# Kernel tuning notes

Measured on AMD Instinct MI355X. Metric: run time of the kernel, lower is better.

## Reference

```python
import jax, jax.numpy as jnp
import numpy as np
from jax import lax


def setup_inputs() -> dict:
    key = jax.random.key(0)
    k1, k2 = jax.random.split(key)
    C, H, W = 64, 224, 224
    C_out, hf, wf = 128, 3, 3
    x = jax.random.normal(k1, (C, H, W), dtype=jnp.float32)
    kernels = jax.random.normal(k2, (C_out, C, hf, wf), dtype=jnp.float32)
    return {"x": x, "kernels": kernels}


def reference(x, kernels):
    # Original builds im2col columns per output pixel then does k_col @ x_col,
    # i.e. a cross-correlation with 'valid' padding and stride 1.
    # lax.conv_general_dilated computes exactly this (no kernel flip).
    stride = 1
    out = lax.conv_general_dilated(
        x[None],                       # (1, C, H, W) NCHW
        kernels,                       # (C_out, C_in, hf, wf) OIHW
        window_strides=(stride, stride),
        padding="VALID",
        dimension_numbers=("NCHW", "OIHW", "NCHW"),
    )
    return out[0]                      # (C_out, H_out, W_out)
```

## Files before the change

### kernel.cpp

```cpp
#include <hip/hip_runtime.h>
#include <hip/hip_bf16.h>


#define H_IN   224
#define W_IN   224
#define C_OUT  128
#define H_OUT  222
#define W_OUT  222
#define XP     226
#define CPAD   72
#define WPAD   72
#define TW     68

typedef __attribute__((ext_vector_type(8))) short bf16x8;
typedef __attribute__((ext_vector_type(4))) float f32x4;

static __device__ __forceinline__ unsigned short f2bs(float f) {
    union { __hip_bfloat16 h; unsigned short u; } cv;
    cv.h = __float2bfloat16(f);
    return cv.u;
}

__global__ __launch_bounds__(256)
void transform_w_kernel(const float* __restrict__ w, __hip_bfloat16* __restrict__ wt)
{
    int idx = blockIdx.x * 256 + threadIdx.x;
    if (idx < 9 * 128 * 64) {
        int ij  = idx >> 13;
        int rem = idx & 8191;
        int co  = rem >> 6;
        int c   = rem & 63;
        wt[idx] = __float2bfloat16(w[(co * 64 + c) * 9 + ij]);
    }
}

__global__ __launch_bounds__(256)
void transpose_x_kernel(const float* __restrict__ x, __hip_bfloat16* __restrict__ xt)
{
    __shared__ __align__(16) unsigned short tile[64 * TW];
    const int h  = blockIdx.y;
    const int w0 = blockIdx.x * 64;
    const int t  = threadIdx.x;

    {
        const int wq = (t & 15) * 4;
        const int c0 = t >> 4;
        #pragma unroll
        for (int p = 0; p < 4; ++p) {
            const int c  = c0 + p * 16;
            const int wg = w0 + wq;
            float4 v = make_float4(0.f, 0.f, 0.f, 0.f);
            if (h < H_IN && wg < W_IN)
                v = *(const float4*)(x + ((size_t)c * H_IN + h) * W_IN + wg);
            ushort4 b;
            b.x = f2bs(v.x); b.y = f2bs(v.y); b.z = f2bs(v.z); b.w = f2bs(v.w);
            *(ushort4*)(tile + c * TW + wq) = b;
        }
    }
    __syncthreads();

    {
        const int wl = t >> 2;
        const int cq = (t & 3) * 16;
        const int wg = w0 + wl;
        if (wg < XP) {
            alignas(16) unsigned short r[16];
            #pragma unroll
            for (int k = 0; k < 16; ++k)
                r[k] = tile[(cq + k) * TW + wl];
            float4* d = (float4*)((unsigned short*)xt + ((size_t)h * XP + wg) * 64 + cq);
            d[0] = ((const float4*)r)[0];
            d[1] = ((const float4*)r)[1];
        }
    }
}

__global__ __launch_bounds__(256)
void conv_mfma_kernel(const __hip_bfloat16* __restrict__ xt,
                      const __hip_bfloat16* __restrict__ wt,
                      float* __restrict__ out)
{
    __shared__ __hip_bfloat16 xs[10 * 18 * CPAD];
    __shared__ __hip_bfloat16 ws[3 * 64 * WPAD];
    const int ow0 = blockIdx.x * 16;
    const int oh0 = blockIdx.y * 8;
    const int co0 = blockIdx.z * 64;
    const int tid = threadIdx.x;

    const int wave = tid >> 6;
    const int lane = tid & 63;
    const int lq   = lane >> 4;
    const int lm   = lane & 15;
    const int r0   = wave * 2;

    for (int q = tid; q < 10 * 18 * 8; q += 256) {
        int sub = q & 7;
        int pix = q >> 3;
        int row = pix / 18;
        int wc  = pix - row * 18;
        *(float4*)(xs + (row * 18 + wc) * CPAD + sub * 8) =
            *(const float4*)(xt + ((oh0 + row) * XP + (ow0 + wc)) * 64 + sub * 8);
    }

    f32x4 acc[2][4] = {};

    #pragma unroll
    for (int i = 0; i < 3; ++i) {
        if (i > 0) __syncthreads();
        #pragma unroll
        for (int k = 0; k < 6; ++k) {
            int q   = k * 256 + tid;
            int jj  = q >> 9;
            int r   = q & 511;
            int co  = r >> 3;
            int sub = r & 7;
            *(float4*)(ws + (jj * 64 + co) * WPAD + sub * 8) =
                *(const float4*)(wt + ((i * 3 + jj) * 128 + co0 + co) * 64 + sub * 8);
        }
        __syncthreads();

        #pragma unroll
        for (int jj = 0; jj < 3; ++jj) {
            bf16x8 afr[2][4];
            #pragma unroll
            for (int t = 0; t < 2; ++t)
                #pragma unroll
                for (int ms = 0; ms < 4; ++ms)
                    afr[t][ms] = *(const bf16x8*)(ws +
                        (jj * 64 + ms * 16 + lm) * WPAD + t * 32 + lq * 8);
            #pragma unroll
            for (int rr = 0; rr < 2; ++rr) {
                #pragma unroll
                for (int t = 0; t < 2; ++t) {
                    bf16x8 bfr = *(const bf16x8*)(xs +
                        ((i + r0 + rr) * 18 + lm + jj) * CPAD + t * 32 + lq * 8);
                    #pragma unroll
                    for (int ms = 0; ms < 4; ++ms)
                        acc[rr][ms] = __builtin_amdgcn_mfma_f32_16x16x32_bf16(
                            afr[t][ms], bfr, acc[rr][ms], 0, 0, 0);
                }
            }
        }
    }

    #pragma unroll
    for (int rr = 0; rr < 2; ++rr) {
        int oh = oh0 + r0 + rr;
        int ow = ow0 + lm;
        if (oh < H_OUT && ow < W_OUT) {
            #pragma unroll
            for (int ms = 0; ms < 4; ++ms) {
                int co = co0 + ms * 16 + lq * 4;
                #pragma unroll
                for (int d = 0; d < 4; ++d)
                    out[(co + d) * (H_OUT * W_OUT) + oh * W_OUT + ow] = acc[rr][ms][d];
            }
        }
    }
}

extern "C" void kernel_launch(void* const* d_in, const int* in_sizes, int n_in,
                              void* d_out, int out_size, void* d_ws, size_t ws_size,
                              hipStream_t stream)
{
    const float* x = (const float*)d_in[0];
    const float* w = (const float*)d_in[1];
    float* out     = (float*)d_out;

    __hip_bfloat16* xt = (__hip_bfloat16*)d_ws;
    __hip_bfloat16* wt = (__hip_bfloat16*)((char*)d_ws + (size_t)XP * XP * 64 * 2);

    transform_w_kernel<<<288, 256, 0, stream>>>(w, wt);
    transpose_x_kernel<<<dim3(4, XP), 256, 0, stream>>>(x, xt);
    conv_mfma_kernel<<<dim3(14, 28, 2), 256, 0, stream>>>(xt, wt, out);
}
```

Before: 88.78 us.

## Switch conv to 32x32x16 MFMA with wider tiles and register-resident weights

Replaces the 16x16x32 bf16 MFMA tiling with 32x32x16 MFMA. Each block now covers 32 output columns instead of 16, halving the grid along width. The weight tile is no longer staged through shared memory: each lane loads its A fragments directly from global memory into registers, which removes the per-tap-row barriers and LDS writes. This raises register pressure and means repeated global or L2 weight reads across blocks.

```diff
diff --git a/kernel.cpp b/kernel.cpp
--- a/kernel.cpp
+++ b/kernel.cpp
@@ -9,11 +9,10 @@
 #define W_OUT  222
 #define XP     226
 #define CPAD   72
-#define WPAD   72
 #define TW     68
 
-typedef __attribute__((ext_vector_type(8))) short bf16x8;
-typedef __attribute__((ext_vector_type(4))) float f32x4;
+typedef __attribute__((ext_vector_type(8)))  short bf16x8;
+typedef __attribute__((ext_vector_type(16))) float f32x16;
 
 static __device__ __forceinline__ unsigned short f2bs(float f) {
     union { __hip_bfloat16 h; unsigned short u; } cv;
@@ -80,80 +79,72 @@
                       const __hip_bfloat16* __restrict__ wt,
                       float* __restrict__ out)
 {
-    __shared__ __hip_bfloat16 xs[10 * 18 * CPAD];
-    __shared__ __hip_bfloat16 ws[3 * 64 * WPAD];
-    const int ow0 = blockIdx.x * 16;
+    __shared__ __hip_bfloat16 xs[10 * 34 * CPAD];
+    const int ow0 = blockIdx.x * 32;
     const int oh0 = blockIdx.y * 8;
     const int co0 = blockIdx.z * 64;
     const int tid = threadIdx.x;
 
+    for (int q = tid; q < 10 * 34 * 8; q += 256) {
+        int sub = q & 7;
+        int pix = q >> 3;
+        int row = pix / 34;
+        int wc  = pix - row * 34;
+        *(float4*)(xs + (row * 34 + wc) * CPAD + sub * 8) =
+            *(const float4*)(xt + ((oh0 + row) * XP + (ow0 + wc)) * 64 + sub * 8);
+    }
+    __syncthreads();
+
     const int wave = tid >> 6;
     const int lane = tid & 63;
-    const int lq   = lane >> 4;
-    const int lm   = lane & 15;
-    const int r0   = wave * 2;
+    const int n    = lane & 31;
+    const int h    = lane >> 5;
 
-    for (int q = tid; q < 10 * 18 * 8; q += 256) {
-        int sub = q & 7;
-        int pix = q >> 3;
-        int row = pix / 18;
-        int wc  = pix - row * 18;
-        *(float4*)(xs + (row * 18 + wc) * CPAD + sub * 8) =
-            *(const float4*)(xt + ((oh0 + row) * XP + (ow0 + wc)) * 64 + sub * 8);
-    }
-
-    f32x4 acc[2][4] = {};
+    f32x16 acc[2][2] = {};
 
     #pragma unroll
     for (int i = 0; i < 3; ++i) {
-        if (i > 0) __syncthreads();
+        bf16x8 afr[3][2][4];
         #pragma unroll
-        for (int k = 0; k < 6; ++k) {
-            int q   = k * 256 + tid;
-            int jj  = q >> 9;
-            int r   = q & 511;
-            int co  = r >> 3;
-            int sub = r & 7;
-            *(float4*)(ws + (jj * 64 + co) * WPAD + sub * 8) =
-                *(const float4*)(wt + ((i * 3 + jj) * 128 + co0 + co) * 64 + sub * 8);
-        }
-        __syncthreads();
+        for (int jj = 0; jj < 3; ++jj)
+            #pragma unroll
+            for (int mi = 0; mi < 2; ++mi)
+                #pragma unroll
+                for (int t = 0; t < 4; ++t)
+                    afr[jj][mi][t] = *(const bf16x8*)(wt +
+                        ((i * 3 + jj) * 128 + co0 + mi * 32 + n) * 64 + t * 16 + h * 8);
 
         #pragma unroll
         for (int jj = 0; jj < 3; ++jj) {
-            bf16x8 afr[2][4];
             #pragma unroll
-            for (int t = 0; t < 2; ++t)
+            for (int t = 0; t < 4; ++t) {
+                bf16x8 bfr[2];
                 #pragma unroll
-                for (int ms = 0; ms < 4; ++ms)
-                    afr[t][ms] = *(const bf16x8*)(ws +
-                        (jj * 64 + ms * 16 + lm) * WPAD + t * 32 + lq * 8);
-            #pragma unroll
-            for (int rr = 0; rr < 2; ++rr) {
+                for (int ni = 0; ni < 2; ++ni)
+                    bfr[ni] = *(const bf16x8*)(xs +
+                        ((wave * 2 + ni + i) * 34 + n + jj) * CPAD + t * 16 + h * 8);
                 #pragma unroll
-                for (int t = 0; t < 2; ++t) {
-                    bf16x8 bfr = *(const bf16x8*)(xs +
-                        ((i + r0 + rr) * 18 + lm + jj) * CPAD + t * 32 + lq * 8);
+                for (int mi = 0; mi < 2; ++mi)
                     #pragma unroll
-                    for (int ms = 0; ms < 4; ++ms)
-                        acc[rr][ms] = __builtin_amdgcn_mfma_f32_16x16x32_bf16(
-                            afr[t][ms], bfr, acc[rr][ms], 0, 0, 0);
-                }
+                    for (int ni = 0; ni < 2; ++ni)
+                        acc[mi][ni] = __builtin_amdgcn_mfma_f32_32x32x16_bf16(
+                            afr[jj][mi][t], bfr[ni], acc[mi][ni], 0, 0, 0);
             }
         }
     }
 
     #pragma unroll
-    for (int rr = 0; rr < 2; ++rr) {
-        int oh = oh0 + r0 + rr;
-        int ow = ow0 + lm;
-        if (oh < H_OUT && ow < W_OUT) {
-            #pragma unroll
-            for (int ms = 0; ms < 4; ++ms) {
-                int co = co0 + ms * 16 + lq * 4;
+    for (int mi = 0; mi < 2; ++mi) {
+        #pragma unroll
+        for (int ni = 0; ni < 2; ++ni) {
+            const int oh = oh0 + wave * 2 + ni;
+            const int ow = ow0 + n;
+            if (oh < H_OUT && ow < W_OUT) {
                 #pragma unroll
-                for (int d = 0; d < 4; ++d)
-                    out[(co + d) * (H_OUT * W_OUT) + oh * W_OUT + ow] = acc[rr][ms][d];
+                for (int r = 0; r < 16; ++r) {
+                    int co = co0 + mi * 32 + (r & 3) + 8 * (r >> 2) + 4 * h;
+                    out[(size_t)co * (H_OUT * W_OUT) + oh * W_OUT + ow] = acc[mi][ni][r];
+                }
             }
         }
     }
@@ -172,5 +163,5 @@
 
     transform_w_kernel<<<288, 256, 0, stream>>>(w, wt);
     transpose_x_kernel<<<dim3(4, XP), 256, 0, stream>>>(x, xt);
-    conv_mfma_kernel<<<dim3(14, 28, 2), 256, 0, stream>>>(xt, wt, out);
+    conv_mfma_kernel<<<dim3(7, 28, 2), 256, 0, stream>>>(xt, wt, out);
 }
```

Measured after the change: 98.14 us. 10.5% more time.
